# Optimization experiments

Hardware: AMD Instinct MI355X
Metric: run time of the kernel (lower is better)

Reference implementation:

```python
import jax, jax.numpy as jnp
import numpy as np

B, Q, K, D, H = 2, 2048, 2048, 1024, 16
HD = D // H  # 64
EPS = 1e-6  # flax LayerNorm default epsilon


def setup_inputs() -> dict:
    key = jax.random.key(0)
    ks = jax.random.split(key, 12)
    s = 1.0 / np.sqrt(D)  # lecun_normal-like scale
    inputs_q = jax.random.normal(ks[0], (B, Q, D), jnp.float32)
    bias = jax.random.normal(ks[1], (B, 1, Q, K), jnp.float32)
    mask = jax.random.randint(ks[2], (B, 1, Q, K), 0, 2).astype(jnp.bool_)
    wq = jax.random.normal(ks[3], (D, H, HD), jnp.float32) * s
    wk = jax.random.normal(ks[4], (D, H, HD), jnp.float32) * s
    wv = jax.random.normal(ks[5], (D, H, HD), jnp.float32) * s
    bq = jnp.zeros((H, HD), jnp.float32)
    bk = jnp.zeros((H, HD), jnp.float32)
    bv = jnp.zeros((H, HD), jnp.float32)
    q_scale = jnp.ones((HD,), jnp.float32)
    k_scale = jnp.ones((HD,), jnp.float32)
    wo = jax.random.normal(ks[6], (H, HD, D), jnp.float32) * s
    bo = jnp.zeros((D,), jnp.float32)
    return dict(inputs_q=inputs_q, bias=bias, mask=mask, wq=wq, bq=bq,
                wk=wk, bk=bk, wv=wv, bv=bv, q_scale=q_scale, k_scale=k_scale,
                wo=wo, bo=bo)


def _layernorm_nobias(x, scale):
    # normalize over last axis (head_dim), no bias, like flax LayerNorm(use_bias=False)
    mean = jnp.mean(x, axis=-1, keepdims=True)
    var = jnp.mean(jnp.square(x - mean), axis=-1, keepdims=True)
    return (x - mean) * jax.lax.rsqrt(var + EPS) * scale


def reference(inputs_q, bias, mask, wq, bq, wk, bk, wv, bv, q_scale, k_scale, wo, bo):
    # QKV projections (self-attention: k and v inputs default to inputs_q)
    q = jnp.einsum('bqd,dhe->bqhe', inputs_q, wq) + bq  # [B,Q,H,HD]
    k = jnp.einsum('bkd,dhe->bkhe', inputs_q, wk) + bk  # [B,K,H,HD]
    v = jnp.einsum('bkd,dhe->bkhe', inputs_q, wv) + bv  # [B,K,H,HD]
    # optional QK layernorm (normalize_qk=True)
    q = _layernorm_nobias(q, q_scale)
    k = _layernorm_nobias(k, k_scale)
    # attention weights
    q = q / jnp.sqrt(jnp.asarray(q.shape[-1], q.dtype))
    attn = jnp.einsum('bqhe,bkhe->bhqk', q, k)  # [B,H,Q,K]
    attn = attn + bias
    big_neg = jnp.finfo(q.dtype).min
    attn = jnp.where(mask, attn, big_neg)
    attn = jax.nn.softmax(attn.astype(jnp.float32), axis=-1).astype(q.dtype)
    # weighted values + output projection
    x = jnp.einsum('bhqk,bkhe->bqhe', attn, v)  # [B,Q,H,HD]
    out = jnp.einsum('bqhe,heo->bqo', x, wo) + bo  # [B,Q,D]
    return out
```

## Files before the change

kernel.cpp:

```cpp
#include <hip/hip_runtime.h>
#include <cstdint>
#include <cstddef>

typedef __bf16 bf16_t;
typedef __bf16 bf16x8 __attribute__((ext_vector_type(8)));
typedef __bf16 bf16x4 __attribute__((ext_vector_type(4)));
typedef _Float16 f16_t;
typedef _Float16 f16x4 __attribute__((ext_vector_type(4)));
typedef float f32x4 __attribute__((ext_vector_type(4)));

constexpr int BB = 2, SS = 2048, DD = 1024, HH = 16, HDIM = 64;
constexpr int BS = BB * SS;
constexpr float LOG2E = 1.4426950408889634f;

__device__ __forceinline__ void glds16(const void* g, void* l) {
  __builtin_amdgcn_global_load_lds((const __attribute__((address_space(1))) void*)g,
                                   (__attribute__((address_space(3))) void*)l, 16, 0, 0);
}

__global__ __launch_bounds__(256) void prep_fused(
    const float* __restrict__ x, const float* __restrict__ wq, const float* __restrict__ wk,
    const float* __restrict__ wv, const float* __restrict__ wo, const float* __restrict__ bias,
    const int* __restrict__ mask, bf16_t* __restrict__ xb, bf16_t* __restrict__ wqkv_t,
    bf16_t* __restrict__ wo_t, f16_t* __restrict__ vmq) {
  __shared__ __align__(16) char smem[18432];
  float (*tile)[65] = (float(*)[65])smem;
  f16_t (*btile)[72] = (f16_t(*)[72])smem;
  int bid = blockIdx.x;
  int t = threadIdx.x;
  if (bid < 4096) {
    int i = bid * 256 + t;
    float4 v = ((const float4*)x)[i];
    union { bf16_t h[4]; uint2 u; } o;
    o.h[0] = (bf16_t)v.x; o.h[1] = (bf16_t)v.y; o.h[2] = (bf16_t)v.z; o.h[3] = (bf16_t)v.w;
    ((uint2*)xb)[i] = o.u;
  } else if (bid < 5120) {
    int id = bid - 4096;
    int which = id >> 8, tr = (id >> 4) & 15, tc = id & 15;
    const float* src = (which == 0) ? wq : (which == 1) ? wk : (which == 2) ? wv : wo;
    bf16_t* dst = (which < 3) ? wqkv_t : wo_t;
    int noff = (which < 3) ? which * 1024 : 0;
#pragma unroll
    for (int p = 0; p < 4; ++p) {
      int e = (p * 256 + t) * 4;
      int r = e >> 6, c = e & 63;
      float4 v = *(const float4*)&src[(size_t)(tr * 64 + r) * 1024 + tc * 64 + c];
      tile[r][c] = v.x; tile[r][c + 1] = v.y; tile[r][c + 2] = v.z; tile[r][c + 3] = v.w;
    }
    __syncthreads();
#pragma unroll
    for (int p = 0; p < 4; ++p) {
      int e = (p * 256 + t) * 4;
      int r = e >> 6, c = e & 63;
      union { bf16_t h[4]; uint2 u; } o;
#pragma unroll
      for (int j = 0; j < 4; ++j) o.h[j] = (bf16_t)tile[c + j][r];
      *(uint2*)&dst[(size_t)(noff + tc * 64 + r) * 1024 + tr * 64 + c] = o.u;
    }
  } else {
    int id = bid - 5120;
    int b = id >> 9, qt = (id >> 5) & 15, kt = id & 31;
    size_t base_in = ((size_t)(b * 2048 + qt * 128)) * 2048 + kt * 64;
#pragma unroll
    for (int p = 0; p < 4; ++p) {
      int c = p * 256 + t;
      int qr = c >> 3, k8 = (c & 7) * 8;
      const float* bp = &bias[base_in + (size_t)qr * 2048 + k8];
      const int* mp = &mask[base_in + (size_t)qr * 2048 + k8];
      float4 b0 = *(const float4*)bp;
      float4 b1 = *(const float4*)(bp + 4);
      int4 m0 = *(const int4*)mp;
      int4 m1 = *(const int4*)(mp + 4);
      union { f16_t h[8]; uint4 u; } o;
      o.h[0] = m0.x ? (f16_t)__builtin_amdgcn_exp2f(b0.x * LOG2E - 8.0f) : (f16_t)0.0f;
      o.h[1] = m0.y ? (f16_t)__builtin_amdgcn_exp2f(b0.y * LOG2E - 8.0f) : (f16_t)0.0f;
      o.h[2] = m0.z ? (f16_t)__builtin_amdgcn_exp2f(b0.z * LOG2E - 8.0f) : (f16_t)0.0f;
      o.h[3] = m0.w ? (f16_t)__builtin_amdgcn_exp2f(b0.w * LOG2E - 8.0f) : (f16_t)0.0f;
      o.h[4] = m1.x ? (f16_t)__builtin_amdgcn_exp2f(b1.x * LOG2E - 8.0f) : (f16_t)0.0f;
      o.h[5] = m1.y ? (f16_t)__builtin_amdgcn_exp2f(b1.y * LOG2E - 8.0f) : (f16_t)0.0f;
      o.h[6] = m1.z ? (f16_t)__builtin_amdgcn_exp2f(b1.z * LOG2E - 8.0f) : (f16_t)0.0f;
      o.h[7] = m1.w ? (f16_t)__builtin_amdgcn_exp2f(b1.w * LOG2E - 8.0f) : (f16_t)0.0f;
      *(uint4*)&btile[qr][k8] = o.u;
    }
    __syncthreads();
    int w = t >> 6, lane = t & 63, lo = lane & 15, quad = lane >> 4;
    size_t obase = ((size_t)(((b * 16 + qt) * 32 + kt) * 16)) * 64;
#pragma unroll
    for (int j = 0; j < 4; ++j) {
      int row = w * 32 + (j >> 1) * 16 + lo;
      int mbl = 2 * (j & 1);
      union { f16_t h[8]; uint4 u; } o;
#pragma unroll
      for (int e = 0; e < 8; ++e)
        o.h[e] = btile[row][(mbl + (e >> 2)) * 16 + quad * 4 + (e & 3)];
      ((uint4*)vmq)[obase + (w * 4 + j) * 64 + lane] = o.u;
    }
  }
}

template <bool OUT_F32, int BNT>
__global__ __launch_bounds__(256) void gemm_bt(const bf16_t* __restrict__ A,
                                               const bf16_t* __restrict__ Bt,
                                               bf16_t* __restrict__ Cb, float* __restrict__ Cf,
                                               const float* __restrict__ bias, int M, int N,
                                               int Kd) {
  constexpr int WNW = BNT / 2;
  constexpr int NFR = WNW / 16;
  __shared__ __align__(16) bf16_t As[128][32];
  __shared__ __align__(16) bf16_t Bs[BNT][32];
  int tid = threadIdx.x;
  int lane = tid & 63, w = tid >> 6;
  int lo = lane & 15, quad = lane >> 4;
  int wm = w >> 1, wn = w & 1;
  int nbx = gridDim.x;
  int nwg = nbx * gridDim.y;
  int lid = blockIdx.y * nbx + blockIdx.x;
  int sid = (lid & 7) * (nwg >> 3) + (lid >> 3);
  int m0 = (sid / nbx) * 128, n0 = (sid % nbx) * BNT;
  int srow = lane >> 2;
  int scol = (lane & 3) * 8;
  f32x4 acc[4][NFR] = {};
  for (int kk = 0; kk < Kd; kk += 32) {
#pragma unroll
    for (int t = 0; t < 2; ++t) {
      int rb = (w * 2 + t) * 16;
      glds16(&A[(size_t)(m0 + rb + srow) * Kd + kk + scol], &As[rb][0]);
      if (rb < BNT) glds16(&Bt[(size_t)(n0 + rb + srow) * Kd + kk + scol], &Bs[rb][0]);
    }
    asm volatile("s_waitcnt vmcnt(0)" ::: "memory");
    __syncthreads();
    bf16x8 am[4], bn[NFR];
#pragma unroll
    for (int i = 0; i < 4; ++i) am[i] = *(const bf16x8*)&As[wm * 64 + i * 16 + lo][quad * 8];
#pragma unroll
    for (int i = 0; i < NFR; ++i) bn[i] = *(const bf16x8*)&Bs[wn * WNW + i * 16 + lo][quad * 8];
#pragma unroll
    for (int mi = 0; mi < 4; ++mi)
#pragma unroll
      for (int ni = 0; ni < NFR; ++ni)
        acc[mi][ni] = __builtin_amdgcn_mfma_f32_16x16x32_bf16(am[mi], bn[ni], acc[mi][ni], 0, 0, 0);
    __syncthreads();
  }
#pragma unroll
  for (int mi = 0; mi < 4; ++mi) {
#pragma unroll
    for (int ni = 0; ni < NFR; ++ni) {
#pragma unroll
      for (int r = 0; r < 4; ++r) {
        int row = m0 + wm * 64 + mi * 16 + quad * 4 + r;
        int col = n0 + wn * WNW + ni * 16 + lo;
        float v = acc[mi][ni][r];
        if (OUT_F32)
          Cf[(size_t)row * N + col] = v + bias[col];
        else
          Cb[(size_t)row * N + col] = (bf16_t)v;
      }
    }
  }
}

__global__ __launch_bounds__(256) void postqkv(const bf16_t* __restrict__ Cqkv,
                                               const float* __restrict__ bq,
                                               const float* __restrict__ bk,
                                               const float* __restrict__ bv,
                                               const float* __restrict__ q_scale,
                                               const float* __restrict__ k_scale,
                                               bf16_t* __restrict__ qb, bf16_t* __restrict__ kb,
                                               f16_t* __restrict__ vt) {
  __shared__ float tile[64][65];
  int bid = blockIdx.x;
  int t = threadIdx.x;
  if (bid < 4096) {
    int mode = bid >> 11;
    int lane = t & 63;
    const float* badd = (mode == 0) ? bq : bk;
    const float* sc = (mode == 0) ? q_scale : k_scale;
    bf16_t* dst = (mode == 0) ? qb : kb;
    int vb = (bid & 2047) * 32 + (t >> 6) * 8;
#pragma unroll
    for (int i = 0; i < 8; ++i) {
      int vec = vb + i;
      int bs = vec >> 4, h = vec & 15;
      int b = bs >> 11, s = bs & 2047;
      float x = (float)Cqkv[(size_t)bs * 3072 + mode * 1024 + h * 64 + lane] + badd[h * 64 + lane];
      float sum = x;
#pragma unroll
      for (int off = 32; off >= 1; off >>= 1) sum += __shfl_xor(sum, off, 64);
      float mean = sum * (1.0f / 64.0f);
      float d = x - mean;
      float vs = d * d;
#pragma unroll
      for (int off = 32; off >= 1; off >>= 1) vs += __shfl_xor(vs, off, 64);
      float var = vs * (1.0f / 64.0f);
      float y = d * rsqrtf(var + 1e-6f) * sc[lane];
      if (mode == 0) y *= 0.125f * LOG2E;
      int el = (mode == 0) ? lane : ((((lane >> 3) ^ (s & 7)) << 3) | (lane & 7));
      dst[(size_t)((b * 16 + h) * 2048 + s) * 64 + el] = (bf16_t)y;
    }
  } else {
    int id2 = bid - 4096;
    int st = id2 & 31, h = (id2 >> 5) & 15, b = id2 >> 9;
#pragma unroll
    for (int p = 0; p < 2; ++p) {
      int e = (p * 256 + t) * 8;
      int r = e >> 6, c = e & 63;
      bf16x8 v8 = *(const bf16x8*)&Cqkv[(size_t)(b * SS + st * 64 + r) * 3072 + 2048 + h * 64 + c];
#pragma unroll
      for (int j = 0; j < 8; ++j) tile[r][c + j] = (float)v8[j] + bv[h * 64 + c + j];
    }
    __syncthreads();
#pragma unroll
    for (int p = 0; p < 2; ++p) {
      int e = (p * 256 + t) * 8;
      int r = e >> 6, c = e & 63;
      union { f16_t h[8]; uint4 u; } o;
#pragma unroll
      for (int j = 0; j < 8; ++j) o.h[j] = (f16_t)tile[c + j][r];
      *(uint4*)&vt[(size_t)((b * HH + h) * HDIM + r) * SS + st * 64 +
                   ((((c >> 3) ^ (r & 7)) << 3))] = o.u;
    }
  }
}

#define ATTN_TILE(KT, CUR, STG, VMC)                                                          \
  {                                                                                           \
    if ((KT) == 31) { asm volatile("s_waitcnt vmcnt(0)" ::: "memory"); }                      \
    else            { asm volatile("s_waitcnt vmcnt(8)" ::: "memory"); }                      \
    __builtin_amdgcn_s_barrier();                                                             \
    if ((KT) + 2 < 32) {                                                                      \
      int k0n = ((KT) + 2) * 64;                                                              \
      _Pragma("unroll") for (int tt = 0; tt < 2; ++tt) {                                      \
        int i = w * 2 + tt;                                                                   \
        int r = i * 8 + (lane >> 3);                                                          \
        glds16(&kbase[(size_t)(k0n + r) * 64 + ((lane & 7) << 3)], (STG) + i * 1024);         \
        glds16(&vbase[(size_t)r * SS + k0n + ((lane & 7) << 3)], (STG) + 8192 + i * 1024);    \
      }                                                                                       \
    }                                                                                         \
    __builtin_amdgcn_s_setprio(1);                                                            \
    bf16x8 ka[4][2];                                                                          \
    _Pragma("unroll") for (int mb = 0; mb < 4; ++mb)                                          \
      _Pragma("unroll") for (int ec = 0; ec < 2; ++ec)                                        \
        ka[mb][ec] = *(const bf16x8*)((CUR) + (mb * 16 + lo) * 128 +                          \
                                      ((((ec << 2) | quad) ^ (lo & 7)) << 4));                \
    f16x4 pf[2][4];                                                                           \
    _Pragma("unroll") for (int qg = 0; qg < 2; ++qg)                                          \
      _Pragma("unroll") for (int mb = 0; mb < 4; ++mb) {                                      \
        f32x4 s = {};                                                                         \
        s = __builtin_amdgcn_mfma_f32_16x16x32_bf16(ka[mb][0], bqf[qg][0], s, 0, 0, 0);       \
        s = __builtin_amdgcn_mfma_f32_16x16x32_bf16(ka[mb][1], bqf[qg][1], s, 0, 0, 0);       \
        f16x4 p4;                                                                             \
        p4[0] = (f16_t)__builtin_amdgcn_exp2f(fminf(s[0], 15.0f));                            \
        p4[1] = (f16_t)__builtin_amdgcn_exp2f(fminf(s[1], 15.0f));                            \
        p4[2] = (f16_t)__builtin_amdgcn_exp2f(fminf(s[2], 15.0f));                            \
        p4[3] = (f16_t)__builtin_amdgcn_exp2f(fminf(s[3], 15.0f));                            \
        pf[qg][mb] = p4 * VMC[qg * 2 + (mb >> 1)].q[mb & 1];                                  \
      }                                                                                       \
    __builtin_amdgcn_s_setprio(0);                                                            \
    if ((KT) + 2 < 32) {           \
      _Pragma("unroll") for (int j = 0; j < 4; ++j)                                           \
        VMC[j].u = vmtile[(size_t)((KT) + 2) * 1024 + j * 64];                                \
    }                                                                                         \
    __builtin_amdgcn_s_setprio(1);                                                            \
    _Pragma("unroll") for (int mb = 0; mb < 4; ++mb) {                                        \
      _Pragma("unroll") for (int eb = 0; eb < 4; ++eb) {                                      \
        f16x4 va = *(const f16x4*)((CUR) + 8192 + (eb * 16 + lo) * 128 +                      \
                                   (((((mb << 1) | (quad >> 1)) ^ (lo & 7)) << 4) |           \
                                    ((quad & 1) << 3)));                                      \
        _Pragma("unroll") for (int qg = 0; qg < 2; ++qg)                                      \
          ot[qg][eb] =                                                                        \
              __builtin_amdgcn_mfma_f32_16x16x16f16(va, pf[qg][mb], ot[qg][eb], 0, 0, 0);     \
      }                                                                                       \
      _Pragma("unroll") for (int qg = 0; qg < 2; ++qg)                                        \
        lacc[qg] = __builtin_amdgcn_mfma_f32_16x16x16f16(ones, pf[qg][mb], lacc[qg], 0, 0, 0);\
    }                                                                                         \
    __builtin_amdgcn_s_setprio(0);                                                            \
  }

__global__ __launch_bounds__(256, 2) void attn_kernel(const bf16_t* __restrict__ qb,
                                                      const bf16_t* __restrict__ kb,
                                                      const f16_t* __restrict__ vt,
                                                      const f16_t* __restrict__ vmq,
                                                      bf16_t* __restrict__ xout) {
  __shared__ __align__(16) char lds[4][16384];
  int tid = threadIdx.x;
  int lane = tid & 63, w = tid >> 6;
  int lo = lane & 15, quad = lane >> 4;
  int qt = blockIdx.x, h = blockIdx.y, b = blockIdx.z;
  size_t headoff = (size_t)(b * HH + h) * SS * HDIM;
  int q0 = qt * 128 + w * 32;
  const bf16_t* kbase = kb + headoff;
  const f16_t* vbase = vt + headoff;
  const uint4* vmtile =
      (const uint4*)vmq + ((size_t)((b * 16 + qt) * 32) * 16 + w * 4) * 64 + lane;

  bf16x8 bqf[2][2];
#pragma unroll
  for (int qg = 0; qg < 2; ++qg)
#pragma unroll
    for (int ec = 0; ec < 2; ++ec)
      bqf[qg][ec] =
          *(const bf16x8*)&qb[headoff + (size_t)(q0 + qg * 16 + lo) * HDIM + ec * 32 + quad * 8];

  f16x4 ones;
#pragma unroll
  for (int j = 0; j < 4; ++j) ones[j] = (f16_t)1.0f;

  f32x4 ot[2][4] = {};
  f32x4 lacc[2] = {};

  union VM { uint4 u; f16x4 q[2]; };
  VM vma[4], vmb[4];

#pragma unroll
  for (int tt = 0; tt < 2; ++tt) {
    int i = w * 2 + tt;
    int r = i * 8 + (lane >> 3);
    glds16(&kbase[(size_t)r * 64 + ((lane & 7) << 3)], lds[0] + i * 1024);
    glds16(&vbase[(size_t)r * SS + ((lane & 7) << 3)], lds[0] + 8192 + i * 1024);
  }
#pragma unroll
  for (int j = 0; j < 4; ++j) vma[j].u = vmtile[j * 64];
#pragma unroll
  for (int tt = 0; tt < 2; ++tt) {
    int i = w * 2 + tt;
    int r = i * 8 + (lane >> 3);
    glds16(&kbase[(size_t)(64 + r) * 64 + ((lane & 7) << 3)], lds[1] + i * 1024);
    glds16(&vbase[(size_t)r * SS + 64 + ((lane & 7) << 3)], lds[1] + 8192 + i * 1024);
  }
#pragma unroll
  for (int j = 0; j < 4; ++j) vmb[j].u = vmtile[1024 + j * 64];

#pragma unroll 1
  for (int kt0 = 0; kt0 < 32; kt0 += 4) {
    ATTN_TILE(kt0 + 0, lds[0], lds[2], vma)
    ATTN_TILE(kt0 + 1, lds[1], lds[3], vmb)
    ATTN_TILE(kt0 + 2, lds[2], lds[0], vma)
    ATTN_TILE(kt0 + 3, lds[3], lds[1], vmb)
  }

#pragma unroll
  for (int qg = 0; qg < 2; ++qg) {
    float rl = 1.0f / lacc[qg][0];
    int q = q0 + qg * 16 + lo;
#pragma unroll
    for (int eb = 0; eb < 4; ++eb) {
      union { bf16_t h4[4]; uint2 u; } o;
#pragma unroll
      for (int r = 0; r < 4; ++r) o.h4[r] = (bf16_t)(ot[qg][eb][r] * rl);
      *(uint2*)&xout[(size_t)(b * SS + q) * DD + h * 64 + eb * 16 + quad * 4] = o.u;
    }
  }
}

extern "C" void kernel_launch(void* const* d_in, const int* in_sizes, int n_in, void* d_out,
                              int out_size, void* d_ws, size_t ws_size, hipStream_t stream) {
  const float* inputs_q = (const float*)d_in[0];
  const float* bias = (const float*)d_in[1];
  const int* mask = (const int*)d_in[2];
  const float* wq = (const float*)d_in[3];
  const float* bq = (const float*)d_in[4];
  const float* wk = (const float*)d_in[5];
  const float* bk = (const float*)d_in[6];
  const float* wv = (const float*)d_in[7];
  const float* bv = (const float*)d_in[8];
  const float* q_scale = (const float*)d_in[9];
  const float* k_scale = (const float*)d_in[10];
  const float* wo = (const float*)d_in[11];
  const float* bo = (const float*)d_in[12];
  float* out = (float*)d_out;

  char* ws = (char*)d_ws;
  bf16_t* wo_t   = (bf16_t*)(ws);
  f16_t*  vmq    = (f16_t*)(ws + ((size_t)2 << 20));
  bf16_t* cqkv   = (bf16_t*)(ws + ((size_t)19 << 20));
  bf16_t* xattn  = (bf16_t*)(ws + ((size_t)19 << 20));
  bf16_t* xb     = (bf16_t*)(ws + ((size_t)43 << 20));
  bf16_t* qb2    = (bf16_t*)(ws + ((size_t)43 << 20));
  bf16_t* wqkv_t = (bf16_t*)(ws + ((size_t)51 << 20));
  bf16_t* kb2    = (bf16_t*)(ws + ((size_t)51 << 20));
  f16_t*  vtb    = (f16_t*)(ws + ((size_t)59 << 20));

  prep_fused<<<6144, 256, 0, stream>>>(inputs_q, wq, wk, wv, wo, bias, mask, xb, wqkv_t, wo_t, vmq);
  gemm_bt<false, 128><<<dim3(24, 32), 256, 0, stream>>>(xb, wqkv_t, cqkv, nullptr, nullptr, BS,
                                                        3072, DD);
  postqkv<<<5120, 256, 0, stream>>>(cqkv, bq, bk, bv, q_scale, k_scale, qb2, kb2, vtb);
  attn_kernel<<<dim3(SS / 128, HH, BB), 256, 0, stream>>>(qb2, kb2, vtb, vmq, xattn);
  gemm_bt<true, 64><<<dim3(16, 32), 256, 0, stream>>>(xattn, wo_t, nullptr, out, bo, BS, 1024, DD);
}
```

Measured before the change: 285.8 us.

## Vectorize QK layernorm, drop exp clamp, remap attention blocks for XCD locality

The q/k layernorm in postqkv now has each thread handle 8 contiguous elements with one 16-byte load and store, reducing the reduction to a 3-step shuffle among 8 lanes instead of 6 full-wave shuffles per vector. The attention softmax no longer clamps scores before exp2, removing a min instruction per element but relying on scores staying within fp16 range. The attention grid is flattened to 1D and block IDs are swizzled so that blocks of the same head land on the same XCD, which is meant to improve K/V cache reuse.

```diff
diff --git a/kernel.cpp b/kernel.cpp
--- a/kernel.cpp
+++ b/kernel.cpp
@@ -171,32 +171,35 @@
   int bid = blockIdx.x;
   int t = threadIdx.x;
   if (bid < 4096) {
-    int mode = bid >> 11;
-    int lane = t & 63;
+    int vec2 = bid * 32 + ((t >> 6) << 3) + ((t & 63) >> 3);
+    int mode = vec2 >> 16;
+    int vec = vec2 & 65535;
+    int bs = vec >> 4, h = vec & 15;
+    int b = bs >> 11, s = bs & 2047;
+    int e0 = (t & 7) * 8;
     const float* badd = (mode == 0) ? bq : bk;
     const float* sc = (mode == 0) ? q_scale : k_scale;
     bf16_t* dst = (mode == 0) ? qb : kb;
-    int vb = (bid & 2047) * 32 + (t >> 6) * 8;
-#pragma unroll
-    for (int i = 0; i < 8; ++i) {
-      int vec = vb + i;
-      int bs = vec >> 4, h = vec & 15;
-      int b = bs >> 11, s = bs & 2047;
-      float x = (float)Cqkv[(size_t)bs * 3072 + mode * 1024 + h * 64 + lane] + badd[h * 64 + lane];
-      float sum = x;
-#pragma unroll
-      for (int off = 32; off >= 1; off >>= 1) sum += __shfl_xor(sum, off, 64);
-      float mean = sum * (1.0f / 64.0f);
-      float d = x - mean;
-      float vs = d * d;
-#pragma unroll
-      for (int off = 32; off >= 1; off >>= 1) vs += __shfl_xor(vs, off, 64);
-      float var = vs * (1.0f / 64.0f);
-      float y = d * rsqrtf(var + 1e-6f) * sc[lane];
-      if (mode == 0) y *= 0.125f * LOG2E;
-      int el = (mode == 0) ? lane : ((((lane >> 3) ^ (s & 7)) << 3) | (lane & 7));
-      dst[(size_t)((b * 16 + h) * 2048 + s) * 64 + el] = (bf16_t)y;
-    }
+    bf16x8 v8 = *(const bf16x8*)&Cqkv[(size_t)bs * 3072 + mode * 1024 + h * 64 + e0];
+    float xv[8];
+    float sum = 0.0f;
+#pragma unroll
+    for (int j = 0; j < 8; ++j) { xv[j] = (float)v8[j] + badd[h * 64 + e0 + j]; sum += xv[j]; }
+#pragma unroll
+    for (int off = 1; off <= 4; off <<= 1) sum += __shfl_xor(sum, off, 64);
+    float mean = sum * (1.0f / 64.0f);
+    float vs = 0.0f;
+#pragma unroll
+    for (int j = 0; j < 8; ++j) { xv[j] -= mean; vs += xv[j] * xv[j]; }
+#pragma unroll
+    for (int off = 1; off <= 4; off <<= 1) vs += __shfl_xor(vs, off, 64);
+    float rstd = rsqrtf(vs * (1.0f / 64.0f) + 1e-6f);
+    if (mode == 0) rstd *= 0.125f * LOG2E;
+    union { bf16_t h[8]; uint4 u; } o;
+#pragma unroll
+    for (int j = 0; j < 8; ++j) o.h[j] = (bf16_t)(xv[j] * rstd * sc[e0 + j]);
+    int ch = (mode == 0) ? (t & 7) : ((t & 7) ^ (s & 7));
+    *(uint4*)&dst[(size_t)((b * 16 + h) * 2048 + s) * 64 + ch * 8] = o.u;
   } else {
     int id2 = bid - 4096;
     int st = id2 & 31, h = (id2 >> 5) & 15, b = id2 >> 9;
@@ -249,10 +252,10 @@
         s = __builtin_amdgcn_mfma_f32_16x16x32_bf16(ka[mb][0], bqf[qg][0], s, 0, 0, 0);       \
         s = __builtin_amdgcn_mfma_f32_16x16x32_bf16(ka[mb][1], bqf[qg][1], s, 0, 0, 0);       \
         f16x4 p4;                                                                             \
-        p4[0] = (f16_t)__builtin_amdgcn_exp2f(fminf(s[0], 15.0f));                            \
-        p4[1] = (f16_t)__builtin_amdgcn_exp2f(fminf(s[1], 15.0f));                            \
-        p4[2] = (f16_t)__builtin_amdgcn_exp2f(fminf(s[2], 15.0f));                            \
-        p4[3] = (f16_t)__builtin_amdgcn_exp2f(fminf(s[3], 15.0f));                            \
+        p4[0] = (f16_t)__builtin_amdgcn_exp2f(s[0]);                                          \
+        p4[1] = (f16_t)__builtin_amdgcn_exp2f(s[1]);                                          \
+        p4[2] = (f16_t)__builtin_amdgcn_exp2f(s[2]);                                          \
+        p4[3] = (f16_t)__builtin_amdgcn_exp2f(s[3]);                                          \
         pf[qg][mb] = p4 * VMC[qg * 2 + (mb >> 1)].q[mb & 1];                                  \
       }                                                                                       \
     __builtin_amdgcn_s_setprio(0);                                                            \
@@ -285,7 +288,9 @@
   int tid = threadIdx.x;
   int lane = tid & 63, w = tid >> 6;
   int lo = lane & 15, quad = lane >> 4;
-  int qt = blockIdx.x, h = blockIdx.y, b = blockIdx.z;
+  int lid = blockIdx.x;
+  int sid = ((lid & 7) << 6) | (lid >> 3);
+  int qt = sid & 15, h = (sid >> 4) & 15, b = sid >> 8;
   size_t headoff = (size_t)(b * HH + h) * SS * HDIM;
   int q0 = qt * 128 + w * 32;
   const bf16_t* kbase = kb + headoff;
@@ -384,6 +389,6 @@
   gemm_bt<false, 128><<<dim3(24, 32), 256, 0, stream>>>(xb, wqkv_t, cqkv, nullptr, nullptr, BS,
                                                         3072, DD);
   postqkv<<<5120, 256, 0, stream>>>(cqkv, bq, bk, bv, q_scale, k_scale, qb2, kb2, vtb);
-  attn_kernel<<<dim3(SS / 128, HH, BB), 256, 0, stream>>>(qb2, kb2, vtb, vmq, xattn);
+  attn_kernel<<<512, 256, 0, stream>>>(qb2, kb2, vtb, vmq, xattn);
   gemm_bt<true, 64><<<dim3(16, 32), 256, 0, stream>>>(xattn, wo_t, nullptr, out, bo, BS, 1024, DD);
 }
```

Result: faster. 271.4 us (-5.0%).
